# Kernel optimization log

Measured on AMD Instinct MI355X. Metric: run time of the kernel, lower is better.

Reference implementation:

```python
import jax, jax.numpy as jnp
import numpy as np

B, T, N, D, NH = 4, 12, 512, 512, 8
DH = D // NH
# Faithful quirk of the original: inside cal_attention, d = K.shape[-1] (the HEAD dim = 64)
# and it divides by sqrt(d / n_h) = sqrt(64/8) = sqrt(8), NOT sqrt(64).
SCALE = 1.0 / np.sqrt(DH / NH).astype(np.float32)
NEG = -1000000000.0


def setup_inputs() -> dict:
    key = jax.random.key(0)
    ks = jax.random.split(key, 9)
    s = 1.0 / np.sqrt(D).astype(np.float32)
    return {
        "V": jax.random.normal(ks[0], (B, T, N, D), jnp.float32),
        "K": jax.random.normal(ks[1], (B, T, N, D), jnp.float32),
        "Q": jax.random.normal(ks[2], (B, T, N, D), jnp.float32),
        "M": jax.random.randint(ks[3], (B, T, N, N), 0, 2, jnp.int32),
        "wx_w": jax.random.normal(ks[4], (3 * D, D), jnp.float32) * s,
        "wx_b": jax.random.normal(ks[5], (3 * D,), jnp.float32) * 0.02,
        "wo_w": jax.random.normal(ks[6], (D, D), jnp.float32) * s,
        "wo_b": jax.random.normal(ks[7], (D,), jnp.float32) * 0.02,
    }


def _split_heads(x):
    # [B,T,N,D] -> [B,T,h,N,d_h]
    b, t, n, _ = x.shape
    return x.reshape(b, t, n, NH, DH).transpose(0, 1, 3, 2, 4)


def reference(V, K, Q, M, wx_w, wx_b, wo_w, wo_b):
    # self-attention branch: Q, K, V all come from wx(Q); inputs V/K are ignored
    wx_o = Q @ wx_w.T + wx_b                      # [B,T,N,3D]
    q, k, v = jnp.split(wx_o, 3, axis=-1)
    q, k, v = _split_heads(q), _split_heads(k), _split_heads(v)  # [B,T,h,N,d_h]
    scores = jnp.einsum("bthqd,bthkd->bthqk", q, k) * SCALE      # [B,T,h,N,N]
    scores = scores + M[:, :, None, :, :].astype(scores.dtype) * NEG
    attn = jax.nn.softmax(scores, axis=-1)
    out = jnp.einsum("bthqk,bthkd->bthqd", attn, v)              # [B,T,h,N,d_h]
    out = out.transpose(0, 1, 3, 2, 4).reshape(B, T, N, D)       # concat heads
    return out @ wo_w.T + wo_b
```

## Files before the change

kernel.cpp:

```cpp
#include <hip/hip_runtime.h>
#include <cstdint>
#include <cstddef>

typedef __bf16 bf16x8_t __attribute__((ext_vector_type(8)));
typedef float f32x4_t __attribute__((ext_vector_type(4)));

#define SCALE 0.3535533905932738f
#define LOG2E 1.4426950408889634f
#define NEG -1000000000.0f

__device__ __forceinline__ unsigned short f2b(float f) {
    unsigned int u = __builtin_bit_cast(unsigned int, f);
    u += 0x7FFFu + ((u >> 16) & 1u);
    return (unsigned short)(u >> 16);
}

__device__ __forceinline__ int swz(int row, int chunk) {
    return row * 64 + (((chunk ^ (row & 7)) << 3));
}

__device__ __forceinline__ void gld16(const void* g, void* l) {
    __builtin_amdgcn_global_load_lds(
        (const __attribute__((address_space(1))) unsigned int*)g,
        (__attribute__((address_space(3))) unsigned int*)l,
        16, 0, 0);
}

__device__ __forceinline__ unsigned int cvt_pk_bf16(float lo, float hi) {
    unsigned int r;
    asm("v_cvt_pk_bf16_f32 %0, %1, %2" : "=v"(r) : "v"(lo), "v"(hi));
    return r;
}

__global__ __launch_bounds__(256) void cvt_kernel(const float* __restrict__ in,
                                                  unsigned short* __restrict__ out,
                                                  int n4) {
    int i = blockIdx.x * 256 + threadIdx.x;
    if (i >= n4) return;
    const float4 f = reinterpret_cast<const float4*>(in)[i];
    ushort4 o;
    o.x = f2b(f.x); o.y = f2b(f.y); o.z = f2b(f.z); o.w = f2b(f.w);
    reinterpret_cast<ushort4*>(out)[i] = o;
}

__global__ __launch_bounds__(256) void gemm_qkv(
    const unsigned short* __restrict__ A,
    const unsigned short* __restrict__ W,
    const float* __restrict__ bias,
    unsigned short* __restrict__ qb,
    unsigned short* __restrict__ kb,
    unsigned short* __restrict__ vT)
{
    __shared__ unsigned short As[128*64];
    __shared__ unsigned short Bs[128*64];
    const int tid = threadIdx.x;
    const int lane = tid & 63;
    const int l15 = lane & 15, lhi = lane >> 4;
    const int wid = tid >> 6, wr = wid >> 1, wc = wid & 1;
    const int bid = blockIdx.x;
    const int sid = (bid & 7) * 288 + (bid >> 3);
    const int m0 = (sid / 12) * 128, n0 = (sid % 12) * 128;
    const int rA = lane >> 3;
    const int sc = (lane & 7) ^ rA;

    f32x4_t acc[4][4] = {};

    for (int k0 = 0; k0 < 512; k0 += 64) {
        __syncthreads();
#pragma unroll
        for (int j = 0; j < 4; ++j) {
            const int ch = 4*wid + j;
            const int gr = ch*8 + rA;
            gld16(&A[(size_t)(m0+gr)*512 + k0 + sc*8], &As[ch*512]);
            gld16(&W[(size_t)(n0+gr)*512 + k0 + sc*8], &Bs[ch*512]);
        }
        asm volatile("s_waitcnt vmcnt(0)" ::: "memory");
        __syncthreads();
#pragma unroll
        for (int kk = 0; kk < 2; ++kk) {
            bf16x8_t af[4], bfr[4];
#pragma unroll
            for (int x = 0; x < 4; ++x) {
                af[x]  = *reinterpret_cast<const bf16x8_t*>(&As[swz(wr*64 + x*16 + l15, kk*4 + lhi)]);
                bfr[x] = *reinterpret_cast<const bf16x8_t*>(&Bs[swz(wc*64 + x*16 + l15, kk*4 + lhi)]);
            }
#pragma unroll
            for (int mi = 0; mi < 4; ++mi)
#pragma unroll
                for (int nj = 0; nj < 4; ++nj)
                    acc[mi][nj] = __builtin_amdgcn_mfma_f32_16x16x32_bf16(af[mi], bfr[nj], acc[mi][nj], 0, 0, 0);
        }
    }

#pragma unroll
    for (int mi = 0; mi < 4; ++mi) {
#pragma unroll
        for (int nj = 0; nj < 4; ++nj) {
            const int gn = n0 + wc*64 + nj*16 + l15;
            const float bi = bias[gn];
            const int which = gn >> 9, hh = (gn >> 6) & 7, dh = gn & 63;
#pragma unroll
            for (int i = 0; i < 4; ++i) {
                const int gm = m0 + wr*64 + mi*16 + lhi*4 + i;
                const int bt = gm >> 9, row = gm & 511;
                const float v = acc[mi][nj][i] + bi;
                const size_t ho = (size_t)bt*8 + hh;
                if (which == 0)      qb[ho*(512*64) + (size_t)row*64 + dh] = f2b(v * (SCALE * LOG2E));
                else if (which == 1) kb[ho*(512*64) + (size_t)row*64 + dh] = f2b(v);
                else                 vT[ho*(64*512) + (size_t)dh*512 + row] = f2b(v);
            }
        }
    }
}

__global__ __launch_bounds__(512, 4) void attn_kernel(
    const unsigned short* __restrict__ qb,
    const unsigned short* __restrict__ kb,
    const unsigned short* __restrict__ vT,
    const int* __restrict__ Mm,
    unsigned short* __restrict__ ob)
{
    __shared__ unsigned short Ks[2][64*64];
    __shared__ unsigned short Vs[2][64*64];
    __shared__ unsigned short Ps[8][32*40];

    const int tid = threadIdx.x;
    const int lane = tid & 63;
    const int w = tid >> 6;
    const int l15 = lane & 15, lhi = lane >> 4;
    const int bid = blockIdx.x;
    const int sid = (bid & 7) * 96 + (bid >> 3);
    const int qt = sid & 1;
    const int h  = (sid >> 1) & 7;
    const int bt = sid >> 4;
    const int q0 = qt*256 + w*32;
    const size_t hoQK = ((size_t)bt*8 + h) * (512*64);
    const size_t hoV  = ((size_t)bt*8 + h) * (64*512);

    const int rA = lane >> 3;
    const int sc = (lane & 7) ^ rA;
    const int trK = w*8 + rA;

    bf16x8_t qf[2][2];
#pragma unroll
    for (int qmi = 0; qmi < 2; ++qmi)
#pragma unroll
        for (int kk = 0; kk < 2; ++kk)
            qf[qmi][kk] = *reinterpret_cast<const bf16x8_t*>(
                &qb[hoQK + (size_t)(q0 + qmi*16 + l15)*64 + kk*32 + lhi*8]);

    bf16x8_t ones;
    {
        uint4 u = {0x3F803F80u, 0x3F803F80u, 0x3F803F80u, 0x3F803F80u};
        ones = __builtin_bit_cast(bf16x8_t, u);
    }

    f32x4_t of[2][4] = {};
    f32x4_t ofl[2] = {};

    const size_t mrow0 = ((size_t)bt*512 + q0 + l15) * 512;

    gld16(&kb[hoQK + (size_t)trK*64 + sc*8],          &Ks[0][w*512]);
    gld16(&vT[hoV + (size_t)(w*8 + rA)*512 + sc*8],   &Vs[0][w*512]);

    for (int kbk = 0; kbk < 8; ++kbk) {
        const int cur = kbk & 1;
        if (kbk < 7) {
            const int t = kbk + 1, nb = cur ^ 1;
            gld16(&kb[hoQK + (size_t)(t*64 + trK)*64 + sc*8],        &Ks[nb][w*512]);
            gld16(&vT[hoV + (size_t)(w*8 + rA)*512 + t*64 + sc*8],   &Vs[nb][w*512]);
            asm volatile("s_waitcnt vmcnt(2)" ::: "memory");
        } else {
            asm volatile("s_waitcnt vmcnt(0)" ::: "memory");
        }
        __syncthreads();

#pragma unroll
        for (int half = 0; half < 2; ++half) {
            bf16x8_t kf[2][2];
#pragma unroll
            for (int knjh = 0; knjh < 2; ++knjh)
#pragma unroll
                for (int kk = 0; kk < 2; ++kk)
                    kf[knjh][kk] = *reinterpret_cast<const bf16x8_t*>(
                        &Ks[cur][swz((half*2 + knjh)*16 + l15, kk*4 + lhi)]);

            int4 mv[2][2];
#pragma unroll
            for (int knjh = 0; knjh < 2; ++knjh)
#pragma unroll
                for (int qmi = 0; qmi < 2; ++qmi)
                    mv[knjh][qmi] = *reinterpret_cast<const int4*>(
                        &Mm[mrow0 + (size_t)(qmi*16)*512 + kbk*64 + (half*2 + knjh)*16 + lhi*4]);

            f32x4_t sa[2][2] = {};
            __builtin_amdgcn_s_setprio(1);
#pragma unroll
            for (int kk = 0; kk < 2; ++kk)
#pragma unroll
                for (int knjh = 0; knjh < 2; ++knjh)
#pragma unroll
                    for (int qmi = 0; qmi < 2; ++qmi)
                        sa[knjh][qmi] = __builtin_amdgcn_mfma_f32_16x16x32_bf16(
                            kf[knjh][kk], qf[qmi][kk], sa[knjh][qmi], 0, 0, 0);
            __builtin_amdgcn_s_setprio(0);

#pragma unroll
            for (int knjh = 0; knjh < 2; ++knjh)
#pragma unroll
                for (int qmi = 0; qmi < 2; ++qmi) {
                    const float p0 = exp2f(fmaf((float)mv[knjh][qmi].x, NEG, sa[knjh][qmi][0]));
                    const float p1 = exp2f(fmaf((float)mv[knjh][qmi].y, NEG, sa[knjh][qmi][1]));
                    const float p2 = exp2f(fmaf((float)mv[knjh][qmi].z, NEG, sa[knjh][qmi][2]));
                    const float p3 = exp2f(fmaf((float)mv[knjh][qmi].w, NEG, sa[knjh][qmi][3]));
                    const unsigned int p01 = cvt_pk_bf16(p0, p1);
                    const unsigned int p23 = cvt_pk_bf16(p2, p3);
                    const int base = (qmi*16 + l15)*40 + knjh*16 + lhi*4;
                    *reinterpret_cast<unsigned int*>(&Ps[w][base])     = p01;
                    *reinterpret_cast<unsigned int*>(&Ps[w][base + 2]) = p23;
                }

            bf16x8_t pf[2];
#pragma unroll
            for (int qmi = 0; qmi < 2; ++qmi)
                pf[qmi] = *reinterpret_cast<const bf16x8_t*>(&Ps[w][(qmi*16 + l15)*40 + lhi*8]);

            bf16x8_t vf[4];
#pragma unroll
            for (int dj = 0; dj < 4; ++dj)
                vf[dj] = *reinterpret_cast<const bf16x8_t*>(&Vs[cur][swz(dj*16 + l15, half*4 + lhi)]);

            __builtin_amdgcn_s_setprio(1);
#pragma unroll
            for (int qmi = 0; qmi < 2; ++qmi) {
                ofl[qmi] = __builtin_amdgcn_mfma_f32_16x16x32_bf16(pf[qmi], ones, ofl[qmi], 0, 0, 0);
#pragma unroll
                for (int dj = 0; dj < 4; ++dj)
                    of[qmi][dj] = __builtin_amdgcn_mfma_f32_16x16x32_bf16(pf[qmi], vf[dj], of[qmi][dj], 0, 0, 0);
            }
            __builtin_amdgcn_s_setprio(0);
        }

        __syncthreads();
    }

#pragma unroll
    for (int qmi = 0; qmi < 2; ++qmi)
#pragma unroll
        for (int i = 0; i < 4; ++i) {
            const int qrow = q0 + qmi*16 + lhi*4 + i;
            const float inv = 1.f / ofl[qmi][i];
#pragma unroll
            for (int dj = 0; dj < 4; ++dj)
                ob[((size_t)bt*512 + qrow)*512 + h*64 + dj*16 + l15] = f2b(of[qmi][dj][i] * inv);
        }
}

__global__ __launch_bounds__(256) void gemm_out(
    const unsigned short* __restrict__ A,
    const unsigned short* __restrict__ W,
    const float* __restrict__ bias,
    float* __restrict__ out)
{
    __shared__ unsigned short As[128*64];
    __shared__ unsigned short Bs[128*64];
    const int tid = threadIdx.x;
    const int lane = tid & 63;
    const int l15 = lane & 15, lhi = lane >> 4;
    const int wid = tid >> 6, wr = wid >> 1, wc = wid & 1;
    const int bid = blockIdx.x;
    const int sid = (bid & 7) * 96 + (bid >> 3);
    const int m0 = (sid / 4) * 128, n0 = (sid % 4) * 128;
    const int rA = lane >> 3;
    const int sc = (lane & 7) ^ rA;

    f32x4_t acc[4][4] = {};

    for (int k0 = 0; k0 < 512; k0 += 64) {
        __syncthreads();
#pragma unroll
        for (int j = 0; j < 4; ++j) {
            const int ch = 4*wid + j;
            const int gr = ch*8 + rA;
            gld16(&A[(size_t)(m0+gr)*512 + k0 + sc*8], &As[ch*512]);
            gld16(&W[(size_t)(n0+gr)*512 + k0 + sc*8], &Bs[ch*512]);
        }
        asm volatile("s_waitcnt vmcnt(0)" ::: "memory");
        __syncthreads();
#pragma unroll
        for (int kk = 0; kk < 2; ++kk) {
            bf16x8_t af[4], bfr[4];
#pragma unroll
            for (int x = 0; x < 4; ++x) {
                af[x]  = *reinterpret_cast<const bf16x8_t*>(&As[swz(wr*64 + x*16 + l15, kk*4 + lhi)]);
                bfr[x] = *reinterpret_cast<const bf16x8_t*>(&Bs[swz(wc*64 + x*16 + l15, kk*4 + lhi)]);
            }
#pragma unroll
            for (int mi = 0; mi < 4; ++mi)
#pragma unroll
                for (int nj = 0; nj < 4; ++nj)
                    acc[mi][nj] = __builtin_amdgcn_mfma_f32_16x16x32_bf16(af[mi], bfr[nj], acc[mi][nj], 0, 0, 0);
        }
    }

#pragma unroll
    for (int mi = 0; mi < 4; ++mi) {
#pragma unroll
        for (int nj = 0; nj < 4; ++nj) {
            const int gn = n0 + wc*64 + nj*16 + l15;
            const float bi = bias[gn];
#pragma unroll
            for (int i = 0; i < 4; ++i) {
                const int gm = m0 + wr*64 + mi*16 + lhi*4 + i;
                out[(size_t)gm*512 + gn] = acc[mi][nj][i] + bi;
            }
        }
    }
}

extern "C" void kernel_launch(void* const* d_in, const int* in_sizes, int n_in,
                              void* d_out, int out_size, void* d_ws, size_t ws_size,
                              hipStream_t stream) {
    (void)in_sizes; (void)n_in; (void)out_size; (void)ws_size;
    const float* Qin = (const float*)d_in[2];
    const int*   Mm  = (const int*)d_in[3];
    const float* wxw = (const float*)d_in[4];
    const float* wxb = (const float*)d_in[5];
    const float* wow = (const float*)d_in[6];
    const float* wob = (const float*)d_in[7];
    float* out = (float*)d_out;

    char* ws = (char*)d_ws;
    const size_t SZ_A  = (size_t)24576*512*2;
    const size_t SZ_WX = (size_t)1536*512*2;
    const size_t SZ_WO = (size_t)512*512*2;
    const size_t SZ_H  = (size_t)48*8*512*64*2;

    unsigned short* Abf  = (unsigned short*)(ws);
    unsigned short* Wxb  = (unsigned short*)(ws + SZ_A);
    unsigned short* Wob  = (unsigned short*)(ws + SZ_A + SZ_WX);
    unsigned short* qb   = (unsigned short*)(ws + SZ_A + SZ_WX + SZ_WO);
    unsigned short* kbuf = (unsigned short*)(ws + SZ_A + SZ_WX + SZ_WO + SZ_H);
    unsigned short* vT   = (unsigned short*)(ws + SZ_A + SZ_WX + SZ_WO + 2*SZ_H);
    unsigned short* attn = Abf;

    cvt_kernel<<<(24576*512/4)/256, 256, 0, stream>>>(Qin, Abf, 24576*512/4);
    cvt_kernel<<<(1536*512/4)/256, 256, 0, stream>>>(wxw, Wxb, 1536*512/4);
    cvt_kernel<<<(512*512/4)/256, 256, 0, stream>>>(wow, Wob, 512*512/4);

    gemm_qkv<<<2304, 256, 0, stream>>>(Abf, Wxb, wxb, qb, kbuf, vT);
    attn_kernel<<<768, 512, 0, stream>>>(qb, kbuf, vT, Mm, attn);
    gemm_out<<<768, 256, 0, stream>>>(attn, Wob, wob, out);
}
```

Before: 198.1 us.

## Double-buffer LDS tiles in QKV and output GEMMs to overlap loads with MFMA

Both projection GEMMs now use two LDS buffers, issuing the next K-tile's global-to-LDS loads before computing on the current tile, so memory latency overlaps MFMA work. It also raises wave priority around the MFMA block with s_setprio. The cost is doubled LDS per block (64KB), which can lower occupancy. A single barrier per iteration appears sufficient because the next prefetch targets the buffer read in the previous iteration, after the sync.

```diff
diff --git a/kernel.cpp b/kernel.cpp
--- a/kernel.cpp
+++ b/kernel.cpp
@@ -51,8 +51,8 @@
     unsigned short* __restrict__ kb,
     unsigned short* __restrict__ vT)
 {
-    __shared__ unsigned short As[128*64];
-    __shared__ unsigned short Bs[128*64];
+    __shared__ unsigned short As[2][128*64];
+    __shared__ unsigned short Bs[2][128*64];
     const int tid = threadIdx.x;
     const int lane = tid & 63;
     const int l15 = lane & 15, lhi = lane >> 4;
@@ -65,32 +65,48 @@
 
     f32x4_t acc[4][4] = {};
 
-    for (int k0 = 0; k0 < 512; k0 += 64) {
-        __syncthreads();
-#pragma unroll
-        for (int j = 0; j < 4; ++j) {
-            const int ch = 4*wid + j;
-            const int gr = ch*8 + rA;
-            gld16(&A[(size_t)(m0+gr)*512 + k0 + sc*8], &As[ch*512]);
-            gld16(&W[(size_t)(n0+gr)*512 + k0 + sc*8], &Bs[ch*512]);
-        }
-        asm volatile("s_waitcnt vmcnt(0)" ::: "memory");
-        __syncthreads();
+#define QKV_STAGE(buf, k0)                                                         \
+    do {                                                                           \
+        _Pragma("unroll")                                                          \
+        for (int j = 0; j < 4; ++j) {                                              \
+            const int ch = 4*wid + j;                                              \
+            const int gr = ch*8 + rA;                                              \
+            gld16(&A[(size_t)(m0+gr)*512 + (k0) + sc*8], &As[buf][ch*512]);        \
+            gld16(&W[(size_t)(n0+gr)*512 + (k0) + sc*8], &Bs[buf][ch*512]);        \
+        }                                                                          \
+    } while (0)
+
+    QKV_STAGE(0, 0);
+    asm volatile("s_waitcnt vmcnt(0)" ::: "memory");
+    __syncthreads();
+
+    int cur = 0;
+#pragma unroll
+    for (int t = 0; t < 8; ++t) {
+        if (t < 7) QKV_STAGE(cur ^ 1, (t+1)*64);
 #pragma unroll
         for (int kk = 0; kk < 2; ++kk) {
             bf16x8_t af[4], bfr[4];
 #pragma unroll
             for (int x = 0; x < 4; ++x) {
-                af[x]  = *reinterpret_cast<const bf16x8_t*>(&As[swz(wr*64 + x*16 + l15, kk*4 + lhi)]);
-                bfr[x] = *reinterpret_cast<const bf16x8_t*>(&Bs[swz(wc*64 + x*16 + l15, kk*4 + lhi)]);
-            }
+                af[x]  = *reinterpret_cast<const bf16x8_t*>(&As[cur][swz(wr*64 + x*16 + l15, kk*4 + lhi)]);
+                bfr[x] = *reinterpret_cast<const bf16x8_t*>(&Bs[cur][swz(wc*64 + x*16 + l15, kk*4 + lhi)]);
+            }
+            __builtin_amdgcn_s_setprio(1);
 #pragma unroll
             for (int mi = 0; mi < 4; ++mi)
 #pragma unroll
                 for (int nj = 0; nj < 4; ++nj)
                     acc[mi][nj] = __builtin_amdgcn_mfma_f32_16x16x32_bf16(af[mi], bfr[nj], acc[mi][nj], 0, 0, 0);
-        }
-    }
+            __builtin_amdgcn_s_setprio(0);
+        }
+        if (t < 7) {
+            asm volatile("s_waitcnt vmcnt(0)" ::: "memory");
+            __syncthreads();
+            cur ^= 1;
+        }
+    }
+#undef QKV_STAGE
 
 #pragma unroll
     for (int mi = 0; mi < 4; ++mi) {
@@ -262,8 +278,8 @@
     const float* __restrict__ bias,
     float* __restrict__ out)
 {
-    __shared__ unsigned short As[128*64];
-    __shared__ unsigned short Bs[128*64];
+    __shared__ unsigned short As[2][128*64];
+    __shared__ unsigned short Bs[2][128*64];
     const int tid = threadIdx.x;
     const int lane = tid & 63;
     const int l15 = lane & 15, lhi = lane >> 4;
@@ -276,32 +292,48 @@
 
     f32x4_t acc[4][4] = {};
 
-    for (int k0 = 0; k0 < 512; k0 += 64) {
-        __syncthreads();
-#pragma unroll
-        for (int j = 0; j < 4; ++j) {
-            const int ch = 4*wid + j;
-            const int gr = ch*8 + rA;
-            gld16(&A[(size_t)(m0+gr)*512 + k0 + sc*8], &As[ch*512]);
-            gld16(&W[(size_t)(n0+gr)*512 + k0 + sc*8], &Bs[ch*512]);
-        }
-        asm volatile("s_waitcnt vmcnt(0)" ::: "memory");
-        __syncthreads();
+#define OUT_STAGE(buf, k0)                                                         \
+    do {                                                                           \
+        _Pragma("unroll")                                                          \
+        for (int j = 0; j < 4; ++j) {                                              \
+            const int ch = 4*wid + j;                                              \
+            const int gr = ch*8 + rA;                                              \
+            gld16(&A[(size_t)(m0+gr)*512 + (k0) + sc*8], &As[buf][ch*512]);        \
+            gld16(&W[(size_t)(n0+gr)*512 + (k0) + sc*8], &Bs[buf][ch*512]);        \
+        }                                                                          \
+    } while (0)
+
+    OUT_STAGE(0, 0);
+    asm volatile("s_waitcnt vmcnt(0)" ::: "memory");
+    __syncthreads();
+
+    int cur = 0;
+#pragma unroll
+    for (int t = 0; t < 8; ++t) {
+        if (t < 7) OUT_STAGE(cur ^ 1, (t+1)*64);
 #pragma unroll
         for (int kk = 0; kk < 2; ++kk) {
             bf16x8_t af[4], bfr[4];
 #pragma unroll
             for (int x = 0; x < 4; ++x) {
-                af[x]  = *reinterpret_cast<const bf16x8_t*>(&As[swz(wr*64 + x*16 + l15, kk*4 + lhi)]);
-                bfr[x] = *reinterpret_cast<const bf16x8_t*>(&Bs[swz(wc*64 + x*16 + l15, kk*4 + lhi)]);
-            }
+                af[x]  = *reinterpret_cast<const bf16x8_t*>(&As[cur][swz(wr*64 + x*16 + l15, kk*4 + lhi)]);
+                bfr[x] = *reinterpret_cast<const bf16x8_t*>(&Bs[cur][swz(wc*64 + x*16 + l15, kk*4 + lhi)]);
+            }
+            __builtin_amdgcn_s_setprio(1);
 #pragma unroll
             for (int mi = 0; mi < 4; ++mi)
 #pragma unroll
                 for (int nj = 0; nj < 4; ++nj)
                     acc[mi][nj] = __builtin_amdgcn_mfma_f32_16x16x32_bf16(af[mi], bfr[nj], acc[mi][nj], 0, 0, 0);
-        }
-    }
+            __builtin_amdgcn_s_setprio(0);
+        }
+        if (t < 7) {
+            asm volatile("s_waitcnt vmcnt(0)" ::: "memory");
+            __syncthreads();
+            cur ^= 1;
+        }
+    }
+#undef OUT_STAGE
 
 #pragma unroll
     for (int mi = 0; mi < 4; ++mi) {
```

Result: faster. 193.5 us (-2.3%).
